# Kernel tuning notes

Hardware: AMD Instinct MI355X
Metric: run time of the kernel (lower is better)

## Reference

```python
import jax, jax.numpy as jnp
import numpy as np

B, C, W, H = 4, 256, 64, 64
CQ = C // 8


def setup_inputs() -> dict:
    key = jax.random.key(0)
    ks = jax.random.split(key, 8)
    s = 1.0 / np.sqrt(C)
    return {
        "x": jax.random.normal(ks[0], (B, C, W, H), dtype=jnp.float32),
        "Wq": jax.random.normal(ks[1], (CQ, C), dtype=jnp.float32) * s,
        "bq": jnp.zeros((CQ,), dtype=jnp.float32),
        "Wk": jax.random.normal(ks[2], (CQ, C), dtype=jnp.float32) * s,
        "bk": jnp.zeros((CQ,), dtype=jnp.float32),
        "Wv": jax.random.normal(ks[3], (C, C), dtype=jnp.float32) * s,
        "bv": jnp.zeros((C,), dtype=jnp.float32),
        "gamma": jnp.zeros((1,), dtype=jnp.float32),
    }


def reference(x, Wq, bq, Wk, bk, Wv, bv, gamma):
    b, c, w, h = x.shape
    n = w * h
    xf = x.reshape(b, c, n)  # [B, C, N] flattened spatial
    # 1x1 convs are channel-wise linear maps
    q = jnp.einsum("dc,bcn->bnd", Wq, xf) + bq  # [B, N, C//8]
    k = jnp.einsum("dc,bcn->bdn", Wk, xf) + bk[None, :, None]  # [B, C//8, N]
    v = jnp.einsum("dc,bcn->bdn", Wv, xf) + bv[None, :, None]  # [B, C, N]
    attn = jax.nn.softmax(jnp.einsum("bnd,bdm->bnm", q, k), axis=-1)  # [B, N, N]
    # out[b, c, n] = sum_m v[b, c, m] * attn[b, n, m]
    out = jnp.einsum("bdm,bnm->bdn", v, attn).reshape(b, c, w, h)
    return gamma[0] * out + x
```

## Files before the change

### kernel.cpp

```cpp
#include <hip/hip_runtime.h>
#include <hip/hip_bf16.h>

#define CC 256
#define NN 4096
#define CQ 32
#define LOG2E 1.4426950408889634f

using short8 = __attribute__((ext_vector_type(8))) short;
using f32x4  = __attribute__((ext_vector_type(4))) float;

static __device__ __forceinline__ short f2bf(float f) {
  __hip_bfloat16 h = __float2bfloat16(f);
  return *reinterpret_cast<short*>(&h);
}

__global__ __launch_bounds__(512, 2) void qkv_kernel(
    const float* __restrict__ x,
    const float* __restrict__ Wq, const float* __restrict__ bq,
    const float* __restrict__ Wk, const float* __restrict__ bk,
    const float* __restrict__ Wv, const float* __restrict__ bv,
    __hip_bfloat16* __restrict__ qb, __hip_bfloat16* __restrict__ kb,
    __hip_bfloat16* __restrict__ vb)
{
  const int b  = blockIdx.y;
  const int n0 = blockIdx.x * 64;
  const int tid = threadIdx.x;
  const int lane = tid & 63;
  const int w = __builtin_amdgcn_readfirstlane(tid >> 6);
  const int l15 = lane & 15, quad = lane >> 4;

  __shared__ __align__(16) short Xs[64][264];
  __shared__ __align__(16) short Vr[8][16][72];

  const int sn = tid & 63, cg8 = tid >> 6;
  const float* xcol = x + (size_t)b*CC*NN + n0 + sn;
#pragma unroll
  for (int it = 0; it < 4; it++) {
    int cbase = it*64 + cg8*8;
    float v[8];
#pragma unroll
    for (int j = 0; j < 8; j++) v[j] = xcol[(size_t)(cbase + j)*NN];
    short8 sv;
#pragma unroll
    for (int j = 0; j < 8; j++) sv[j] = f2bf(v[j]);
    *reinterpret_cast<short8*>(&Xs[sn][cbase]) = sv;
  }
  __syncthreads();

#define QKV_TILE(T) { \
    const int t_ = (T); \
    const float* wr; \
    { int R = t_*16 + l15; \
      if (t_ < 2)      wr = Wq + (size_t)R*CC; \
      else if (t_ < 4) wr = Wk + (size_t)(R-32)*CC; \
      else             wr = Wv + (size_t)(R-64)*CC; } \
    short8 Af[8]; \
    _Pragma("unroll") \
    for (int kc = 0; kc < 8; kc++) { \
      float4 fa = *(const float4*)(wr + kc*32 + quad*8); \
      float4 fc = *(const float4*)(wr + kc*32 + quad*8 + 4); \
      short8 o; \
      o[0]=f2bf(fa.x); o[1]=f2bf(fa.y); o[2]=f2bf(fa.z); o[3]=f2bf(fa.w); \
      o[4]=f2bf(fc.x); o[5]=f2bf(fc.y); o[6]=f2bf(fc.z); o[7]=f2bf(fc.w); \
      Af[kc] = o; \
    } \
    f32x4 ac0 = {0.f,0.f,0.f,0.f}, ac1 = {0.f,0.f,0.f,0.f}; \
    f32x4 ac2 = {0.f,0.f,0.f,0.f}, ac3 = {0.f,0.f,0.f,0.f}; \
    _Pragma("unroll") \
    for (int kc = 0; kc < 8; kc++) { \
      short8 B0 = *(const short8*)(&Xs[     l15][kc*32 + quad*8]); \
      short8 B1 = *(const short8*)(&Xs[16 + l15][kc*32 + quad*8]); \
      short8 B2 = *(const short8*)(&Xs[32 + l15][kc*32 + quad*8]); \
      short8 B3 = *(const short8*)(&Xs[48 + l15][kc*32 + quad*8]); \
      ac0 = __builtin_amdgcn_mfma_f32_16x16x32_bf16(Af[kc], B0, ac0, 0,0,0); \
      ac1 = __builtin_amdgcn_mfma_f32_16x16x32_bf16(Af[kc], B1, ac1, 0,0,0); \
      ac2 = __builtin_amdgcn_mfma_f32_16x16x32_bf16(Af[kc], B2, ac2, 0,0,0); \
      ac3 = __builtin_amdgcn_mfma_f32_16x16x32_bf16(Af[kc], B3, ac3, 0,0,0); \
    } \
    if (t_ < 2) { \
      int d0 = t_*16; \
      _Pragma("unroll") \
      for (int r = 0; r < 4; r++) { \
        int d = d0 + quad*4 + r; float bb = bq[d]; \
        qb[(size_t)b*NN*CQ + (size_t)(n0      + l15)*CQ + d] = __float2bfloat16(LOG2E*(ac0[r] + bb)); \
        qb[(size_t)b*NN*CQ + (size_t)(n0 + 16 + l15)*CQ + d] = __float2bfloat16(LOG2E*(ac1[r] + bb)); \
        qb[(size_t)b*NN*CQ + (size_t)(n0 + 32 + l15)*CQ + d] = __float2bfloat16(LOG2E*(ac2[r] + bb)); \
        qb[(size_t)b*NN*CQ + (size_t)(n0 + 48 + l15)*CQ + d] = __float2bfloat16(LOG2E*(ac3[r] + bb)); \
      } \
    } else if (t_ < 4) { \
      int d0 = (t_-2)*16; \
      _Pragma("unroll") \
      for (int r = 0; r < 4; r++) { \
        int d = d0 + quad*4 + r; float bb = bk[d]; \
        kb[(size_t)b*NN*CQ + (size_t)(n0      + l15)*CQ + d] = __float2bfloat16(ac0[r] + bb); \
        kb[(size_t)b*NN*CQ + (size_t)(n0 + 16 + l15)*CQ + d] = __float2bfloat16(ac1[r] + bb); \
        kb[(size_t)b*NN*CQ + (size_t)(n0 + 32 + l15)*CQ + d] = __float2bfloat16(ac2[r] + bb); \
        kb[(size_t)b*NN*CQ + (size_t)(n0 + 48 + l15)*CQ + d] = __float2bfloat16(ac3[r] + bb); \
      } \
    } else { \
      int rv0 = (t_-4)*16; \
      _Pragma("unroll") \
      for (int r = 0; r < 4; r++) { \
        float bb = bv[rv0 + quad*4 + r]; \
        Vr[w][quad*4 + r][     l15] = f2bf(ac0[r] + bb); \
        Vr[w][quad*4 + r][16 + l15] = f2bf(ac1[r] + bb); \
        Vr[w][quad*4 + r][32 + l15] = f2bf(ac2[r] + bb); \
        Vr[w][quad*4 + r][48 + l15] = f2bf(ac3[r] + bb); \
      } \
      int row = lane >> 2, cb = (lane & 3)*16; \
      short8 t0 = *(const short8*)(&Vr[w][row][cb]); \
      short8 t1 = *(const short8*)(&Vr[w][row][cb + 8]); \
      *(short8*)(vb + ((size_t)b*CC + rv0 + row)*NN + n0 + cb)     = t0; \
      *(short8*)(vb + ((size_t)b*CC + rv0 + row)*NN + n0 + cb + 8) = t1; \
    } }

  QKV_TILE(2*w);
  QKV_TILE(2*w + 1);
  if (w < 4) { QKV_TILE(16 + w); }
#undef QKV_TILE
}

__global__ __launch_bounds__(512, 2) void attn_kernel(
    const __hip_bfloat16* __restrict__ qb, const __hip_bfloat16* __restrict__ kb,
    const __hip_bfloat16* __restrict__ vb,
    const float* __restrict__ x, const float* __restrict__ gamma,
    float* __restrict__ out)
{
  const int Bk = blockIdx.x;
  const int b = (Bk & 7) >> 1;
  const int n0 = ((Bk >> 3)*2 + (Bk & 1)) * 64;
  const int tid = threadIdx.x;
  const int lane = tid & 63;
  const int w = __builtin_amdgcn_readfirstlane(tid >> 6);
  const int sg = w & 3;
  const int mh = w >> 2;
  const int l15 = lane & 15, quad = lane >> 4;

  __shared__ __align__(16) short Vsp[8][64][40];
  __shared__ __align__(16) short Ps[2][2][64][40];
  __shared__ float Lbuf2[2][64];

  const short* qbase = (const short*)qb + (size_t)b*NN*CQ;
  const short* kbase = (const short*)kb + (size_t)b*NN*CQ;
  const short* vbase = (const short*)vb + (size_t)b*CC*NN;

  short8 aq = *(const short8*)(qbase + (size_t)(n0 + sg*16 + l15)*CQ + quad*8);

  const int vrow = lane >> 2, vch = lane & 3;
  const short* vwave = vbase + (size_t)(sg*64)*NN + mh*32 + vch*8;

  short8 nv0, nv1, nv2, nv3, kf0, kf1, nk0, nk1;
  {
    const short* vp = vwave + (size_t)vrow*NN;
    nv0 = *(const short8*)(vp);
    nv1 = *(const short8*)(vp + (size_t)16*NN);
    nv2 = *(const short8*)(vp + (size_t)32*NN);
    nv3 = *(const short8*)(vp + (size_t)48*NN);
  }
  kf0 = *(const short8*)(kbase + (size_t)(mh*32 +      l15)*CQ + quad*8);
  kf1 = *(const short8*)(kbase + (size_t)(mh*32 + 16 + l15)*CQ + quad*8);
  *(short8*)(&Vsp[w][vrow     ][vch*8]) = nv0;
  *(short8*)(&Vsp[w][vrow + 16][vch*8]) = nv1;
  *(short8*)(&Vsp[w][vrow + 32][vch*8]) = nv2;
  *(short8*)(&Vsp[w][vrow + 48][vch*8]) = nv3;

  f32x4 acc[4][4];
#pragma unroll
  for (int cg = 0; cg < 4; cg++)
#pragma unroll
    for (int ng = 0; ng < 4; ng++) acc[cg][ng] = (f32x4){0.f,0.f,0.f,0.f};
  float lsum[4] = {0.f,0.f,0.f,0.f};

  for (int T = 0; T < 64; T++) {
    if (T < 63) {
      const short* vp = vwave + (size_t)vrow*NN + (T+1)*64;
      nv0 = *(const short8*)(vp);
      nv1 = *(const short8*)(vp + (size_t)16*NN);
      nv2 = *(const short8*)(vp + (size_t)32*NN);
      nv3 = *(const short8*)(vp + (size_t)48*NN);
      nk0 = *(const short8*)(kbase + (size_t)((T+1)*64 + mh*32 +      l15)*CQ + quad*8);
      nk1 = *(const short8*)(kbase + (size_t)((T+1)*64 + mh*32 + 16 + l15)*CQ + quad*8);
    }

    f32x4 z = {0.f,0.f,0.f,0.f};
    f32x4 S0 = __builtin_amdgcn_mfma_f32_16x16x32_bf16(aq, kf0, z, 0,0,0);
    f32x4 S1 = __builtin_amdgcn_mfma_f32_16x16x32_bf16(aq, kf1, z, 0,0,0);
    const int pb = T & 1;
#pragma unroll
    for (int r = 0; r < 4; r++) {
      float e0 = __builtin_amdgcn_exp2f(S0[r]);
      float e1 = __builtin_amdgcn_exp2f(S1[r]);
      lsum[r] += e0 + e1;
      Ps[pb][mh][sg*16 + quad*4 + r][     l15] = f2bf(e0);
      Ps[pb][mh][sg*16 + quad*4 + r][16 + l15] = f2bf(e1);
    }
    __syncthreads();

    short8 ap0 = *(const short8*)(&Ps[pb][mh][     l15][quad*8]);
    short8 ap1 = *(const short8*)(&Ps[pb][mh][16 + l15][quad*8]);
    short8 ap2 = *(const short8*)(&Ps[pb][mh][32 + l15][quad*8]);
    short8 ap3 = *(const short8*)(&Ps[pb][mh][48 + l15][quad*8]);
#pragma unroll
    for (int cg = 0; cg < 4; cg++) {
      short8 av = *(const short8*)(&Vsp[w][cg*16 + l15][quad*8]);
      acc[cg][0] = __builtin_amdgcn_mfma_f32_16x16x32_bf16(av, ap0, acc[cg][0], 0,0,0);
      acc[cg][1] = __builtin_amdgcn_mfma_f32_16x16x32_bf16(av, ap1, acc[cg][1], 0,0,0);
      acc[cg][2] = __builtin_amdgcn_mfma_f32_16x16x32_bf16(av, ap2, acc[cg][2], 0,0,0);
      acc[cg][3] = __builtin_amdgcn_mfma_f32_16x16x32_bf16(av, ap3, acc[cg][3], 0,0,0);
    }

    if (T < 63) {
      *(short8*)(&Vsp[w][vrow     ][vch*8]) = nv0;
      *(short8*)(&Vsp[w][vrow + 16][vch*8]) = nv1;
      *(short8*)(&Vsp[w][vrow + 32][vch*8]) = nv2;
      *(short8*)(&Vsp[w][vrow + 48][vch*8]) = nv3;
      kf0 = nk0; kf1 = nk1;
    }
  }

#pragma unroll
  for (int r = 0; r < 4; r++) {
    float s = lsum[r];
    s += __shfl_xor(s, 1); s += __shfl_xor(s, 2);
    s += __shfl_xor(s, 4); s += __shfl_xor(s, 8);
    if (l15 == 0) Lbuf2[mh][sg*16 + quad*4 + r] = s;
  }

  float* poolf = reinterpret_cast<float*>(&Vsp[0][0][0]);
  __syncthreads();
#pragma unroll
  for (int g = 0; g < 2; g++) {
    if (mh == 1 && (sg >> 1) == g) {
#pragma unroll
      for (int cg = 0; cg < 4; cg++)
#pragma unroll
        for (int ng = 0; ng < 4; ng++)
#pragma unroll
          for (int r = 0; r < 4; r++)
            poolf[(sg & 1)*4096 + (cg*16 + quad*4 + r)*64 + ng*16 + l15] = acc[cg][ng][r];
    }
    __syncthreads();
    if (mh == 0 && (sg >> 1) == g) {
#pragma unroll
      for (int cg = 0; cg < 4; cg++)
#pragma unroll
        for (int ng = 0; ng < 4; ng++)
#pragma unroll
          for (int r = 0; r < 4; r++)
            acc[cg][ng][r] += poolf[(sg & 1)*4096 + (cg*16 + quad*4 + r)*64 + ng*16 + l15];
    }
    __syncthreads();
  }

  if (mh == 0) {
    const float gm = gamma[0];
    float Lv[4];
#pragma unroll
    for (int ng = 0; ng < 4; ng++)
      Lv[ng] = 1.0f / (Lbuf2[0][ng*16 + l15] + Lbuf2[1][ng*16 + l15]);
#pragma unroll
    for (int cg = 0; cg < 4; cg++) {
#pragma unroll
      for (int ng = 0; ng < 4; ng++) {
#pragma unroll
        for (int r = 0; r < 4; r++) {
          size_t idx = ((size_t)b*CC + sg*64 + cg*16 + quad*4 + r)*NN + n0 + ng*16 + l15;
          out[idx] = gm * acc[cg][ng][r] * Lv[ng] + x[idx];
        }
      }
    }
  }
}

extern "C" void kernel_launch(void* const* d_in, const int* in_sizes, int n_in,
                              void* d_out, int out_size, void* d_ws, size_t ws_size,
                              hipStream_t stream) {
  const float* x     = (const float*)d_in[0];
  const float* Wq    = (const float*)d_in[1];
  const float* bq    = (const float*)d_in[2];
  const float* Wk    = (const float*)d_in[3];
  const float* bk    = (const float*)d_in[4];
  const float* Wv    = (const float*)d_in[5];
  const float* bv    = (const float*)d_in[6];
  const float* gamma = (const float*)d_in[7];
  float* out = (float*)d_out;

  char* ws = (char*)d_ws;
  if (ws_size < (10u << 20)) return;
  __hip_bfloat16* qb = (__hip_bfloat16*)(ws);
  __hip_bfloat16* kb = (__hip_bfloat16*)(ws + (1u << 20));
  __hip_bfloat16* vb = (__hip_bfloat16*)(ws + (2u << 20));

  qkv_kernel<<<dim3(64, 4), 512, 0, stream>>>(x, Wq, bq, Wk, bk, Wv, bv, qb, kb, vb);
  attn_kernel<<<dim3(256), 512, 0, stream>>>(qb, kb, vb, x, gamma, out);
}
```

Baseline: 156.1 us.

## Retile attention to 32-query blocks with direct V loads and no cross-wave reduction

The attention kernel now handles 32 query rows per block instead of 64 and launches 512 blocks. Each wave owns 32 channels and splits the key dimension into four quarters of 128 keys per step. V fragments are loaded straight from global memory into registers instead of being staged in per-wave LDS buffers, and the final cross-wave accumulator reduction through LDS is removed. P is stored as packed bf16 pairs in one LDS buffer, and the launch bound asks for four blocks per CU. The V store in the QKV kernel also now writes packed 32-bit pairs. In exchange, V is re-read from global or cache by more blocks, and the explicit next-tile prefetch is gone.

```diff
diff --git a/kernel.cpp b/kernel.cpp
--- a/kernel.cpp
+++ b/kernel.cpp
@@ -12,6 +12,10 @@
 static __device__ __forceinline__ short f2bf(float f) {
   __hip_bfloat16 h = __float2bfloat16(f);
   return *reinterpret_cast<short*>(&h);
+}
+static __device__ __forceinline__ unsigned short bf16u(float f) {
+  __hip_bfloat16 h = __float2bfloat16(f);
+  return *reinterpret_cast<unsigned short*>(&h);
 }
 
 __global__ __launch_bounds__(512, 2) void qkv_kernel(
@@ -99,13 +103,14 @@
       } \
     } else { \
       int rv0 = (t_-4)*16; \
+      unsigned int* vru = reinterpret_cast<unsigned int*>(&Vr[w][0][0]);  \
       _Pragma("unroll") \
       for (int r = 0; r < 4; r++) { \
         float bb = bv[rv0 + quad*4 + r]; \
-        Vr[w][quad*4 + r][     l15] = f2bf(ac0[r] + bb); \
-        Vr[w][quad*4 + r][16 + l15] = f2bf(ac1[r] + bb); \
-        Vr[w][quad*4 + r][32 + l15] = f2bf(ac2[r] + bb); \
-        Vr[w][quad*4 + r][48 + l15] = f2bf(ac3[r] + bb); \
+        unsigned int p01 = (unsigned int)bf16u(ac0[r] + bb) | ((unsigned int)bf16u(ac1[r] + bb) << 16); \
+        unsigned int p23 = (unsigned int)bf16u(ac2[r] + bb) | ((unsigned int)bf16u(ac3[r] + bb) << 16); \
+        vru[(quad*4 + r)*36 + l15]      = p01;   \
+        vru[(quad*4 + r)*36 + 16 + l15] = p23;   \
       } \
       int row = lane >> 2, cb = (lane & 3)*16; \
       short8 t0 = *(const short8*)(&Vr[w][row][cb]); \
@@ -120,25 +125,24 @@
 #undef QKV_TILE
 }
 
-__global__ __launch_bounds__(512, 2) void attn_kernel(
+__global__ __launch_bounds__(512, 4) void attn_kernel(
     const __hip_bfloat16* __restrict__ qb, const __hip_bfloat16* __restrict__ kb,
     const __hip_bfloat16* __restrict__ vb,
     const float* __restrict__ x, const float* __restrict__ gamma,
     float* __restrict__ out)
 {
   const int Bk = blockIdx.x;
-  const int b = (Bk & 7) >> 1;
-  const int n0 = ((Bk >> 3)*2 + (Bk & 1)) * 64;
+  const int b  = (Bk & 7) >> 1;
+  const int n0 = ((Bk >> 3)*2 + (Bk & 1)) * 32;
   const int tid = threadIdx.x;
   const int lane = tid & 63;
   const int w = __builtin_amdgcn_readfirstlane(tid >> 6);
-  const int sg = w & 3;
-  const int mh = w >> 2;
+  const int sg = w & 1;
+  const int mq = w >> 1;
   const int l15 = lane & 15, quad = lane >> 4;
 
-  __shared__ __align__(16) short Vsp[8][64][40];
-  __shared__ __align__(16) short Ps[2][2][64][40];
-  __shared__ float Lbuf2[2][64];
+  __shared__ unsigned int PsU[2][32][68];
+  __shared__ float Lbuf[4][32];
 
   const short* qbase = (const short*)qb + (size_t)b*NN*CQ;
   const short* kbase = (const short*)kb + (size_t)b*NN*CQ;
@@ -146,76 +150,57 @@
 
   short8 aq = *(const short8*)(qbase + (size_t)(n0 + sg*16 + l15)*CQ + quad*8);
 
-  const int vrow = lane >> 2, vch = lane & 3;
-  const short* vwave = vbase + (size_t)(sg*64)*NN + mh*32 + vch*8;
-
-  short8 nv0, nv1, nv2, nv3, kf0, kf1, nk0, nk1;
-  {
-    const short* vp = vwave + (size_t)vrow*NN;
-    nv0 = *(const short8*)(vp);
-    nv1 = *(const short8*)(vp + (size_t)16*NN);
-    nv2 = *(const short8*)(vp + (size_t)32*NN);
-    nv3 = *(const short8*)(vp + (size_t)48*NN);
-  }
-  kf0 = *(const short8*)(kbase + (size_t)(mh*32 +      l15)*CQ + quad*8);
-  kf1 = *(const short8*)(kbase + (size_t)(mh*32 + 16 + l15)*CQ + quad*8);
-  *(short8*)(&Vsp[w][vrow     ][vch*8]) = nv0;
-  *(short8*)(&Vsp[w][vrow + 16][vch*8]) = nv1;
-  *(short8*)(&Vsp[w][vrow + 32][vch*8]) = nv2;
-  *(short8*)(&Vsp[w][vrow + 48][vch*8]) = nv3;
-
-  f32x4 acc[4][4];
-#pragma unroll
-  for (int cg = 0; cg < 4; cg++)
-#pragma unroll
-    for (int ng = 0; ng < 4; ng++) acc[cg][ng] = (f32x4){0.f,0.f,0.f,0.f};
+  f32x4 acc[2][2];
+#pragma unroll
+  for (int cg = 0; cg < 2; cg++)
+#pragma unroll
+    for (int ng = 0; ng < 2; ng++) acc[cg][ng] = (f32x4){0.f,0.f,0.f,0.f};
   float lsum[4] = {0.f,0.f,0.f,0.f};
 
-  for (int T = 0; T < 64; T++) {
-    if (T < 63) {
-      const short* vp = vwave + (size_t)vrow*NN + (T+1)*64;
-      nv0 = *(const short8*)(vp);
-      nv1 = *(const short8*)(vp + (size_t)16*NN);
-      nv2 = *(const short8*)(vp + (size_t)32*NN);
-      nv3 = *(const short8*)(vp + (size_t)48*NN);
-      nk0 = *(const short8*)(kbase + (size_t)((T+1)*64 + mh*32 +      l15)*CQ + quad*8);
-      nk1 = *(const short8*)(kbase + (size_t)((T+1)*64 + mh*32 + 16 + l15)*CQ + quad*8);
-    }
+  for (int T = 0; T < 32; T++) {
+    const int pb = T & 1;
+    const int mT = T*128 + mq*32;
+
+    short8 kf0 = *(const short8*)(kbase + (size_t)(mT      + l15)*CQ + quad*8);
+    short8 kf1 = *(const short8*)(kbase + (size_t)(mT + 16 + l15)*CQ + quad*8);
 
     f32x4 z = {0.f,0.f,0.f,0.f};
     f32x4 S0 = __builtin_amdgcn_mfma_f32_16x16x32_bf16(aq, kf0, z, 0,0,0);
     f32x4 S1 = __builtin_amdgcn_mfma_f32_16x16x32_bf16(aq, kf1, z, 0,0,0);
-    const int pb = T & 1;
 #pragma unroll
     for (int r = 0; r < 4; r++) {
       float e0 = __builtin_amdgcn_exp2f(S0[r]);
       float e1 = __builtin_amdgcn_exp2f(S1[r]);
       lsum[r] += e0 + e1;
-      Ps[pb][mh][sg*16 + quad*4 + r][     l15] = f2bf(e0);
-      Ps[pb][mh][sg*16 + quad*4 + r][16 + l15] = f2bf(e1);
+      PsU[pb][sg*16 + quad*4 + r][mq*16 + l15] =
+          (unsigned int)bf16u(e0) | ((unsigned int)bf16u(e1) << 16);
     }
+
+    short8 av[2][4];
+#pragma unroll
+    for (int cg = 0; cg < 2; cg++)
+#pragma unroll
+      for (int kq = 0; kq < 4; kq++)
+        av[cg][kq] = *(const short8*)(
+            vbase + (size_t)(w*32 + cg*16 + l15)*NN + T*128 + kq*32 + quad*8);
+
     __syncthreads();
 
-    short8 ap0 = *(const short8*)(&Ps[pb][mh][     l15][quad*8]);
-    short8 ap1 = *(const short8*)(&Ps[pb][mh][16 + l15][quad*8]);
-    short8 ap2 = *(const short8*)(&Ps[pb][mh][32 + l15][quad*8]);
-    short8 ap3 = *(const short8*)(&Ps[pb][mh][48 + l15][quad*8]);
-#pragma unroll
-    for (int cg = 0; cg < 4; cg++) {
-      short8 av = *(const short8*)(&Vsp[w][cg*16 + l15][quad*8]);
-      acc[cg][0] = __builtin_amdgcn_mfma_f32_16x16x32_bf16(av, ap0, acc[cg][0], 0,0,0);
-      acc[cg][1] = __builtin_amdgcn_mfma_f32_16x16x32_bf16(av, ap1, acc[cg][1], 0,0,0);
-      acc[cg][2] = __builtin_amdgcn_mfma_f32_16x16x32_bf16(av, ap2, acc[cg][2], 0,0,0);
-      acc[cg][3] = __builtin_amdgcn_mfma_f32_16x16x32_bf16(av, ap3, acc[cg][3], 0,0,0);
-    }
-
-    if (T < 63) {
-      *(short8*)(&Vsp[w][vrow     ][vch*8]) = nv0;
-      *(short8*)(&Vsp[w][vrow + 16][vch*8]) = nv1;
-      *(short8*)(&Vsp[w][vrow + 32][vch*8]) = nv2;
-      *(short8*)(&Vsp[w][vrow + 48][vch*8]) = nv3;
-      kf0 = nk0; kf1 = nk1;
-    }
+    short8 ap[2][4];
+#pragma unroll
+    for (int ng = 0; ng < 2; ng++)
+#pragma unroll
+      for (int kq = 0; kq < 4; kq++)
+        ap[ng][kq] = *(const short8*)(&PsU[pb][ng*16 + l15][kq*16 + quad*4]);
+
+#pragma unroll
+    for (int cg = 0; cg < 2; cg++)
+#pragma unroll
+      for (int ng = 0; ng < 2; ng++)
+#pragma unroll
+        for (int kq = 0; kq < 4; kq++)
+          acc[cg][ng] = __builtin_amdgcn_mfma_f32_16x16x32_bf16(
+              av[cg][kq], ap[ng][kq], acc[cg][ng], 0,0,0);
   }
 
 #pragma unroll
@@ -223,50 +208,24 @@
     float s = lsum[r];
     s += __shfl_xor(s, 1); s += __shfl_xor(s, 2);
     s += __shfl_xor(s, 4); s += __shfl_xor(s, 8);
-    if (l15 == 0) Lbuf2[mh][sg*16 + quad*4 + r] = s;
-  }
-
-  float* poolf = reinterpret_cast<float*>(&Vsp[0][0][0]);
+    if (l15 == 0) Lbuf[mq][sg*16 + quad*4 + r] = s;
+  }
   __syncthreads();
-#pragma unroll
-  for (int g = 0; g < 2; g++) {
-    if (mh == 1 && (sg >> 1) == g) {
-#pragma unroll
-      for (int cg = 0; cg < 4; cg++)
-#pragma unroll
-        for (int ng = 0; ng < 4; ng++)
-#pragma unroll
-          for (int r = 0; r < 4; r++)
-            poolf[(sg & 1)*4096 + (cg*16 + quad*4 + r)*64 + ng*16 + l15] = acc[cg][ng][r];
-    }
-    __syncthreads();
-    if (mh == 0 && (sg >> 1) == g) {
-#pragma unroll
-      for (int cg = 0; cg < 4; cg++)
-#pragma unroll
-        for (int ng = 0; ng < 4; ng++)
-#pragma unroll
-          for (int r = 0; r < 4; r++)
-            acc[cg][ng][r] += poolf[(sg & 1)*4096 + (cg*16 + quad*4 + r)*64 + ng*16 + l15];
-    }
-    __syncthreads();
-  }
-
-  if (mh == 0) {
-    const float gm = gamma[0];
-    float Lv[4];
-#pragma unroll
-    for (int ng = 0; ng < 4; ng++)
-      Lv[ng] = 1.0f / (Lbuf2[0][ng*16 + l15] + Lbuf2[1][ng*16 + l15]);
-#pragma unroll
-    for (int cg = 0; cg < 4; cg++) {
-#pragma unroll
-      for (int ng = 0; ng < 4; ng++) {
-#pragma unroll
-        for (int r = 0; r < 4; r++) {
-          size_t idx = ((size_t)b*CC + sg*64 + cg*16 + quad*4 + r)*NN + n0 + ng*16 + l15;
-          out[idx] = gm * acc[cg][ng][r] * Lv[ng] + x[idx];
-        }
+
+  const float gm = gamma[0];
+  float Lv[2];
+#pragma unroll
+  for (int ng = 0; ng < 2; ng++)
+    Lv[ng] = 1.0f / (Lbuf[0][ng*16 + l15] + Lbuf[1][ng*16 + l15] +
+                     Lbuf[2][ng*16 + l15] + Lbuf[3][ng*16 + l15]);
+#pragma unroll
+  for (int cg = 0; cg < 2; cg++) {
+#pragma unroll
+    for (int ng = 0; ng < 2; ng++) {
+#pragma unroll
+      for (int r = 0; r < 4; r++) {
+        size_t idx = ((size_t)b*CC + w*32 + cg*16 + quad*4 + r)*NN + n0 + ng*16 + l15;
+        out[idx] = gm * acc[cg][ng][r] * Lv[ng] + x[idx];
       }
     }
   }
@@ -292,5 +251,5 @@
   __hip_bfloat16* vb = (__hip_bfloat16*)(ws + (2u << 20));
 
   qkv_kernel<<<dim3(64, 4), 512, 0, stream>>>(x, Wq, bq, Wk, bk, Wv, bv, qb, kb, vb);
-  attn_kernel<<<dim3(256), 512, 0, stream>>>(qb, kb, vb, x, gamma, out);
-}
+  attn_kernel<<<dim3(512), 512, 0, stream>>>(qb, kb, vb, x, gamma, out);
+}
```

New measurement: 224.4 us. 43.7% more time.
